# Kernel optimization log

Hardware: AMD Instinct MI355X
Metric: run time of the kernel (lower is better)

The kernel has to match this reference:

```python
import jax, jax.numpy as jnp
import numpy as np

N = 20000
E = 640000
H, C = 4, 64
L = 3
B = 16
EPS = 1e-5


def setup_inputs() -> dict:
    key = jax.random.key(0)
    ks = jax.random.split(key, 12)
    x = jax.random.normal(ks[0], (N, 256), dtype=jnp.float32)
    edge_index = jax.random.randint(ks[1], (2, E), 0, N, dtype=jnp.int64)
    batch = jnp.sort(jax.random.randint(ks[2], (N,), 0, B, dtype=jnp.int64))
    s = 0.05
    return {
        "x": x,
        "edge_index": edge_index,
        "batch": batch,
        "Wl": jax.random.normal(ks[3], (L, 256, H * C), dtype=jnp.float32) * s,
        "bl": jnp.zeros((L, H * C), dtype=jnp.float32),
        "Wr": jax.random.normal(ks[4], (L, 256, H * C), dtype=jnp.float32) * s,
        "br": jnp.zeros((L, H * C), dtype=jnp.float32),
        "att": jax.random.normal(ks[5], (L, H, C), dtype=jnp.float32) * s,
        "conv_bias": jnp.zeros((L, H * C), dtype=jnp.float32),
        "prelu_a": jnp.full((L,), 0.25, dtype=jnp.float32),
        "norm_w": jnp.ones((H * C,), dtype=jnp.float32),
        "norm_b": jnp.zeros((H * C,), dtype=jnp.float32),
        "norm_alpha": jnp.ones((H * C,), dtype=jnp.float32),
        "fc_W": jax.random.normal(ks[6], (H * C, 128), dtype=jnp.float32) * s,
        "fc_b": jnp.zeros((128,), dtype=jnp.float32),
    }


def graph_norm(h, w, b, alpha):
    # GraphNorm with batch=None: all rows form one segment (as in source forward)
    mean = jnp.mean(h, axis=0, keepdims=True)
    shifted = h - alpha * mean
    var = jnp.mean(shifted * shifted, axis=0, keepdims=True)
    return w * shifted / jnp.sqrt(var + EPS) + b


def gatv2_layer(h, src, dst, Wl, bl, Wr, br, att, bias):
    xl = (h @ Wl + bl).reshape(N, H, C)  # source transform
    xr = (h @ Wr + br).reshape(N, H, C)  # target transform
    m = jax.nn.leaky_relu(xl[src] + xr[dst], negative_slope=0.2)  # [Etot,H,C]
    e = jnp.einsum("ehc,hc->eh", m, att)  # [Etot,H]
    emax = jax.ops.segment_max(e, dst, num_segments=N)  # self-loops guarantee coverage
    ex = jnp.exp(e - emax[dst])
    denom = jax.ops.segment_sum(ex, dst, num_segments=N)
    alpha = ex / denom[dst]
    out = jax.ops.segment_sum(alpha[:, :, None] * xl[src], dst, num_segments=N)
    return out.reshape(N, H * C) + bias


def reference(x, edge_index, batch, Wl, bl, Wr, br, att, conv_bias, prelu_a,
              norm_w, norm_b, norm_alpha, fc_W, fc_b):
    loop = jnp.arange(N, dtype=edge_index.dtype)
    src = jnp.concatenate([edge_index[0], loop])  # add self-loops (PyG default)
    dst = jnp.concatenate([edge_index[1], loop])
    h = x
    for l in range(L):
        h = gatv2_layer(h, src, dst, Wl[l], bl[l], Wr[l], br[l], att[l], conv_bias[l])
        h = graph_norm(h, norm_w, norm_b, norm_alpha)
        h = jnp.where(h >= 0, h, prelu_a[l] * h)  # PReLU; dropout is identity in eval
    pooled = jax.ops.segment_sum(h, batch, num_segments=B)  # global_add_pool
    pooled = graph_norm(pooled, norm_w, norm_b, norm_alpha)  # shared norm reused after pool
    return pooled @ fc_W + fc_b
```

## Files before the change

kernel.cpp:

```cpp
#include <hip/hip_runtime.h>
#include <math.h>

#define N_NODES 20000
#define N_EDGES 640000
#define ETOT (N_EDGES + N_NODES)
#define HC 256
#define NLAYER 3
#define NBATCH 16
#define GEPS 1e-5f
#define NSLOT 64
#define L2E 1.44269504f

typedef unsigned short u16;
typedef unsigned int u32;
typedef __attribute__((ext_vector_type(8))) short short8;
typedef __attribute__((ext_vector_type(4))) float floatx4;

__device__ __forceinline__ u16 f2bf(float f) {
    u32 u = __float_as_uint(f);
    u32 r = (u + 0x7FFFu + ((u >> 16) & 1u)) >> 16;
    return (u16)r;
}

__device__ __forceinline__ float4 bf2f4(uint2 u) {
    float4 r;
    r.x = __uint_as_float(u.x << 16);
    r.y = __uint_as_float(u.x & 0xFFFF0000u);
    r.z = __uint_as_float(u.y << 16);
    r.w = __uint_as_float(u.y & 0xFFFF0000u);
    return r;
}

__device__ __forceinline__ float dpp_red16(float x) {
    x += __int_as_float(__builtin_amdgcn_update_dpp(0, __float_as_int(x), 0xB1, 0xF, 0xF, true));
    x += __int_as_float(__builtin_amdgcn_update_dpp(0, __float_as_int(x), 0x4E, 0xF, 0xF, true));
    x += __int_as_float(__builtin_amdgcn_update_dpp(0, __float_as_int(x), 0x141, 0xF, 0xF, true));
    x += __int_as_float(__builtin_amdgcn_update_dpp(0, __float_as_int(x), 0x140, 0xF, 0xF, true));
    return x;
}



__global__ __launch_bounds__(256) void prep(const float* __restrict__ x, u16* __restrict__ xbf,
                                            const float* __restrict__ Wl, const float* __restrict__ Wr,
                                            u16* __restrict__ WT, uint4* __restrict__ zbase, int zq) {
    __shared__ float T[32][33];
    int b = blockIdx.x, tid = threadIdx.x;
    if (b < 1250) {
        int rt = b;
        int wid = tid >> 6, lane = tid & 63;
        int row = rt * 16 + (lane & 15);
        int q8 = (lane >> 4) * 8;
        #pragma unroll
        for (int kk = 0; kk < 2; ++kk) {
            int kt = wid + kk * 4;
            int kcol = kt * 32 + q8;
            const float4* px = (const float4*)(x + (size_t)row * 256 + kcol);
            float4 a = px[0], c = px[1];
            u16 o[8] = {f2bf(a.x), f2bf(a.y), f2bf(a.z), f2bf(a.w),
                        f2bf(c.x), f2bf(c.y), f2bf(c.z), f2bf(c.w)};
            *(uint4*)(xbf + (((size_t)rt * 8 + kt) * 64 + lane) * 8) = *(const uint4*)o;
        }
    } else if (b < 1634) {
        int bi = b - 1250;
        int kb = bi & 7;
        int nb = (bi >> 3) & 15;
        int l = bi >> 7;
        int n0 = nb * 32, k0 = kb * 32;
        const float* W = ((n0 < 256) ? Wl : Wr) + (size_t)l * 65536;
        int nn0 = n0 & 255;
        int tx = tid & 31, ty = tid >> 5;
        #pragma unroll
        for (int i = 0; i < 4; ++i)
            T[ty + i * 8][tx] = W[(size_t)(k0 + ty + i * 8) * 256 + nn0 + tx];
        __syncthreads();
        int lane = tid & 63, jp = (tid >> 6) & 1, cl = tid >> 7;
        int ct = n0 / 16 + cl;
        u16 o4[4];
        #pragma unroll
        for (int jj = 0; jj < 4; ++jj)
            o4[jj] = f2bf(T[(lane >> 4) * 8 + jp * 4 + jj][cl * 16 + (lane & 15)]);
        u16* outw = WT + (size_t)l * 131072;
        *(uint2*)(outw + (((size_t)ct * 8 + kb) * 64 + lane) * 8 + jp * 4) = *(const uint2*)o4;
    } else {
        uint4 z = make_uint4(0, 0, 0, 0);
        for (int i = (b - 1634) * 256 + tid; i < zq; i += 120 * 256) zbase[i] = z;
    }
}


__global__ void count_deg(const int* __restrict__ dst, int* __restrict__ deg) {
    int e = blockIdx.x * 256 + threadIdx.x;
    if (e < N_EDGES) atomicAdd(&deg[dst[e]], 1);
}

__global__ __launch_bounds__(1024) void scan_excl(int* __restrict__ data, int* __restrict__ cursor) {
    __shared__ int wsum[16];
    int t = threadIdx.x, lane = t & 63, wid = t >> 6;
    int i0 = t * 20;
    int d[20];
    int tot = 0;
    #pragma unroll
    for (int j = 0; j < 20; ++j) {
        int i = i0 + j;
        int v = (i < N_NODES) ? (data[i] + 1) : 0;
        d[j] = v;
        tot += v;
    }
    int x = tot;
    #pragma unroll
    for (int off = 1; off < 64; off <<= 1) {
        int tmp = __shfl_up(x, off);
        if (lane >= off) x += tmp;
    }
    if (lane == 63) wsum[wid] = x;
    __syncthreads();
    if (t == 0) {
        int run = 0;
        #pragma unroll
        for (int w = 0; w < 16; ++w) { int tv = wsum[w]; wsum[w] = run; run += tv; }
    }
    __syncthreads();
    int run = wsum[wid] + x - tot;
    #pragma unroll
    for (int j = 0; j < 20; ++j) {
        int i = i0 + j;
        if (i < N_NODES) { data[i] = run; cursor[i] = run; }
        run += d[j];
    }
    if (t == 0) data[N_NODES] = ETOT;
}

__global__ void scatter_edges(const int* __restrict__ src, const int* __restrict__ dst,
                              int* __restrict__ cursor, int* __restrict__ col) {
    int t = blockIdx.x * 256 + threadIdx.x;
    if (t < N_NODES) {
        int p = atomicAdd(&cursor[t], 1);
        col[p] = t;
    } else if (t < N_NODES + N_EDGES) {
        int e = t - N_NODES;
        int p = atomicAdd(&cursor[dst[e]], 1);
        col[p] = src[e];
    }
}


__global__ __launch_bounds__(256, 1) void gemm_mfma(
    const u16* __restrict__ At, const u16* __restrict__ WTt,
    const float* __restrict__ b0, const float* __restrict__ b1,
    u16* __restrict__ xlb, u16* __restrict__ xrb) {
    __shared__ u16 tile[32][520];
    int row0 = blockIdx.x * 64;
    int tid = threadIdx.x;
    int wave = tid >> 6, lane = tid & 63;
    int quad = lane >> 4, l16 = lane & 15;
    int rt0 = row0 >> 4;
    int ct0 = wave * 8;

    floatx4 acc[4][8] = {};
    const u16* pA[4];
    const u16* pB[8];
    #pragma unroll
    for (int mi = 0; mi < 4; ++mi) {
        int rt = min(rt0 + mi, 1249);
        pA[mi] = At + (size_t)rt * 4096 + lane * 8;
    }
    #pragma unroll
    for (int ni = 0; ni < 8; ++ni)
        pB[ni] = WTt + (size_t)(ct0 + ni) * 4096 + lane * 8;

    #pragma unroll
    for (int kt = 0; kt < 8; ++kt) {
        short8 af[4], bf[8];
        #pragma unroll
        for (int mi = 0; mi < 4; ++mi) af[mi] = *(const short8*)(pA[mi] + kt * 512);
        #pragma unroll
        for (int ni = 0; ni < 8; ++ni) bf[ni] = *(const short8*)(pB[ni] + kt * 512);
        #pragma unroll
        for (int mi = 0; mi < 4; ++mi)
            #pragma unroll
            for (int ni = 0; ni < 8; ++ni)
                acc[mi][ni] = __builtin_amdgcn_mfma_f32_16x16x32_bf16(af[mi], bf[ni], acc[mi][ni], 0, 0, 0);
    }

    float bv[8];
    #pragma unroll
    for (int ni = 0; ni < 8; ++ni) {
        int c = wave * 128 + ni * 16 + l16;
        bv[ni] = (c < 256) ? b0[c] : b1[c - 256];
    }

    #pragma unroll
    for (int pass = 0; pass < 2; ++pass) {
        #pragma unroll
        for (int mi = 0; mi < 2; ++mi) {
            int lrow = mi * 16 + quad * 4;
            #pragma unroll
            for (int ni = 0; ni < 8; ++ni) {
                int c = wave * 128 + ni * 16 + l16;
                #pragma unroll
                for (int r = 0; r < 4; ++r)
                    tile[lrow + r][c] = f2bf(acc[pass * 2 + mi][ni][r] + bv[ni]);
            }
        }
        __syncthreads();
        #pragma unroll
        for (int iter = 0; iter < 8; ++iter) {
            int lrow = iter * 4 + wave;
            int gr = row0 + pass * 32 + lrow;
            if (gr < N_NODES) {
                if (lane < 32)
                    *(uint4*)(xlb + (size_t)gr * 256 + lane * 8) = *(const uint4*)&tile[lrow][lane * 8];
                else
                    *(uint4*)(xrb + (size_t)gr * 256 + (lane - 32) * 8) = *(const uint4*)&tile[lrow][256 + (lane - 32) * 8];
            }
        }
        __syncthreads();
    }
}


__global__ __launch_bounds__(256) void gat_agg(
    const u16* __restrict__ xlb, const u16* __restrict__ xrb,
    const int* __restrict__ rowptr, const int* __restrict__ col,
    const float* __restrict__ att_l, const float* __restrict__ bias_l,
    u16* __restrict__ hB, float* __restrict__ slot) {
    __shared__ float sred[4][520];
    int wid = threadIdx.x >> 6, lane = threadIdx.x & 63;
    int node = blockIdx.x * 4 + wid;
    const uint2* xl2 = (const uint2*)xlb;
    float4 attv = ((const float4*)att_l)[lane];
    attv.x *= L2E; attv.y *= L2E; attv.z *= L2E; attv.w *= L2E;
    float4 xrv = bf2f4(((const uint2*)xrb)[(size_t)node * 64 + lane]);
    int beg = rowptr[node], end = rowptr[node + 1];

    float denom = 0.f;
    float4 acc = make_float4(0.f, 0.f, 0.f, 0.f);

    int j = beg;
    for (; j + 8 <= end; j += 8) {
        int s[8];
        uint2 raw[8];
        float4 a[8];
        float p[8];
        #pragma unroll
        for (int u = 0; u < 8; ++u) s[u] = col[j + u];
        #pragma unroll
        for (int u = 0; u < 8; ++u) raw[u] = xl2[(size_t)s[u] * 64 + lane];
        #pragma unroll
        for (int u = 0; u < 8; ++u) {
            a[u] = bf2f4(raw[u]);
            float vx = a[u].x + xrv.x, vy = a[u].y + xrv.y;
            float vz = a[u].z + xrv.z, vw = a[u].w + xrv.w;
            vx = fmaxf(vx, 0.2f * vx);
            vy = fmaxf(vy, 0.2f * vy);
            vz = fmaxf(vz, 0.2f * vz);
            vw = fmaxf(vw, 0.2f * vw);
            p[u] = vx * attv.x + vy * attv.y + vz * attv.z + vw * attv.w;
        }
        #pragma unroll
        for (int u = 0; u < 8; ++u) p[u] = dpp_red16(p[u]);
        #pragma unroll
        for (int u = 0; u < 8; ++u) {
            float w = exp2f(p[u]);
            denom += w;
            acc.x += w * a[u].x; acc.y += w * a[u].y;
            acc.z += w * a[u].z; acc.w += w * a[u].w;
        }
    }
    for (; j < end; ++j) {
        int s = col[j];
        float4 a = bf2f4(xl2[(size_t)s * 64 + lane]);
        float vx = a.x + xrv.x, vy = a.y + xrv.y;
        float vz = a.z + xrv.z, vw = a.w + xrv.w;
        vx = fmaxf(vx, 0.2f * vx);
        vy = fmaxf(vy, 0.2f * vy);
        vz = fmaxf(vz, 0.2f * vz);
        vw = fmaxf(vw, 0.2f * vw);
        float p = vx * attv.x + vy * attv.y + vz * attv.z + vw * attv.w;
        p = dpp_red16(p);
        float w = exp2f(p);
        denom += w;
        acc.x += w * a.x; acc.y += w * a.y; acc.z += w * a.z; acc.w += w * a.w;
    }

    float inv = 1.f / denom;
    float4 b4 = ((const float4*)bias_l)[lane];
    float4 o;
    o.x = acc.x * inv + b4.x; o.y = acc.y * inv + b4.y;
    o.z = acc.z * inv + b4.z; o.w = acc.w * inv + b4.w;
    u16 ob[4] = {f2bf(o.x), f2bf(o.y), f2bf(o.z), f2bf(o.w)};
    ((uint2*)hB)[(size_t)node * 64 + lane] = *(const uint2*)ob;

    int cb2 = lane * 4;
    sred[wid][cb2 + 0] = o.x; sred[wid][cb2 + 1] = o.y;
    sred[wid][cb2 + 2] = o.z; sred[wid][cb2 + 3] = o.w;
    sred[wid][256 + cb2 + 0] = o.x * o.x; sred[wid][256 + cb2 + 1] = o.y * o.y;
    sred[wid][256 + cb2 + 2] = o.z * o.z; sred[wid][256 + cb2 + 3] = o.w * o.w;
    __syncthreads();
    int t = threadIdx.x;
    #pragma unroll
    for (int h = 0; h < 2; ++h) {
        int idx = t + h * 256;
        float s = sred[0][idx] + sred[1][idx] + sred[2][idx] + sred[3][idx];
        atomicAdd(&slot[(blockIdx.x & (NSLOT - 1)) * 512 + idx], s);
    }
}


__global__ __launch_bounds__(256) void fin_stats(const float* __restrict__ slot,
                                                 const float* __restrict__ nw, const float* __restrict__ nb,
                                                 const float* __restrict__ na,
                                                 float* __restrict__ wcbb) {
    int c = threadIdx.x;
    float sum = 0.f, sq = 0.f;
    for (int s = 0; s < NSLOT; ++s) {
        sum += slot[s * 512 + c];
        sq += slot[s * 512 + 256 + c];
    }
    const float invn = 1.f / (float)N_NODES;
    float mean = sum * invn, Eh2 = sq * invn;
    float a = na[c];
    float var = Eh2 - (2.f * a - a * a) * mean * mean;
    float wc = nw[c] * rsqrtf(var + GEPS);
    wcbb[c] = wc;
    wcbb[256 + c] = nb[c] - a * mean * wc;
}


__global__ __launch_bounds__(256) void norm_prelu(const u16* __restrict__ hB, u16* __restrict__ hbfT,
                                                  const float* __restrict__ wcbb,
                                                  const float* __restrict__ pa, int l) {
    int rt = blockIdx.x;
    int wid = threadIdx.x >> 6, lane = threadIdx.x & 63;
    float ap = pa[l];
    int row = rt * 16 + (lane & 15);
    int q8 = (lane >> 4) * 8;
    #pragma unroll
    for (int kk = 0; kk < 2; ++kk) {
        int kt = wid + kk * 4;
        int kcol = kt * 32 + q8;
        uint4 raw = *(const uint4*)(hB + (size_t)row * 256 + kcol);
        float4 a = bf2f4(make_uint2(raw.x, raw.y));
        float4 b = bf2f4(make_uint2(raw.z, raw.w));
        float4 wc0 = *(const float4*)&wcbb[kcol];
        float4 wc1 = *(const float4*)&wcbb[kcol + 4];
        float4 bb0 = *(const float4*)&wcbb[256 + kcol];
        float4 bb1 = *(const float4*)&wcbb[256 + kcol + 4];
        a.x = a.x * wc0.x + bb0.x; a.y = a.y * wc0.y + bb0.y;
        a.z = a.z * wc0.z + bb0.z; a.w = a.w * wc0.w + bb0.w;
        b.x = b.x * wc1.x + bb1.x; b.y = b.y * wc1.y + bb1.y;
        b.z = b.z * wc1.z + bb1.z; b.w = b.w * wc1.w + bb1.w;
        a.x = fmaxf(a.x, ap * a.x); a.y = fmaxf(a.y, ap * a.y);
        a.z = fmaxf(a.z, ap * a.z); a.w = fmaxf(a.w, ap * a.w);
        b.x = fmaxf(b.x, ap * b.x); b.y = fmaxf(b.y, ap * b.y);
        b.z = fmaxf(b.z, ap * b.z); b.w = fmaxf(b.w, ap * b.w);
        u16 o[8] = {f2bf(a.x), f2bf(a.y), f2bf(a.z), f2bf(a.w),
                    f2bf(b.x), f2bf(b.y), f2bf(b.z), f2bf(b.w)};
        *(uint4*)(hbfT + (((size_t)rt * 8 + kt) * 64 + lane) * 8) = *(const uint4*)o;
    }
}


__global__ __launch_bounds__(256) void pool_kernel(const u16* __restrict__ hB,
                                                   const int* __restrict__ batch,
                                                   const float* __restrict__ slots2,
                                                   const float* __restrict__ nw, const float* __restrict__ nb,
                                                   const float* __restrict__ na, const float* __restrict__ pa,
                                                   float* __restrict__ pooled) {
    __shared__ float accs[NBATCH][256];
    int c = threadIdx.x;
    float sum = 0.f, sq = 0.f;
    for (int s = 0; s < NSLOT; ++s) {
        sum += slots2[s * 512 + c];
        sq += slots2[s * 512 + 256 + c];
    }
    const float invn = 1.f / (float)N_NODES;
    float mean = sum * invn, Eh2 = sq * invn;
    float a = na[c];
    float var = Eh2 - (2.f * a - a * a) * mean * mean;
    float wc = nw[c] * rsqrtf(var + GEPS);
    float bb = nb[c] - a * mean * wc;
    float ap = pa[2];

    #pragma unroll
    for (int b = 0; b < NBATCH; ++b) accs[b][c] = 0.f;
    int r0 = blockIdx.x * 100;
    int r1 = min(N_NODES, r0 + 100);
    for (int i = r0; i < r1; ++i) {
        float v = __uint_as_float(((u32)hB[(size_t)i * 256 + c]) << 16);
        v = v * wc + bb;
        v = fmaxf(v, ap * v);
        accs[batch[i]][c] += v;
    }
    int bmin = batch[r0], bmax = batch[r1 - 1];
    for (int b = bmin; b <= bmax; ++b) atomicAdd(&pooled[b * 256 + c], accs[b][c]);
}


__global__ __launch_bounds__(256) void poolnorm_fc(const float* __restrict__ pooled,
                                                   const float* __restrict__ nw, const float* __restrict__ nb,
                                                   const float* __restrict__ na,
                                                   const float* __restrict__ fcW, const float* __restrict__ fcb,
                                                   float* __restrict__ out) {
    __shared__ float pn[256];
    __shared__ float part[128];
    int b = blockIdx.x;
    int c = threadIdx.x;
    float mean = 0.f, sq = 0.f;
    #pragma unroll
    for (int i = 0; i < NBATCH; ++i) {
        float v = pooled[i * 256 + c];
        mean += v; sq += v * v;
    }
    mean *= (1.f / NBATCH); sq *= (1.f / NBATCH);
    float a = na[c];
    float var = sq - (2.f * a - a * a) * mean * mean;
    float wc = nw[c] * rsqrtf(var + GEPS);
    float bb = nb[c] - a * mean * wc;
    pn[c] = pooled[b * 256 + c] * wc + bb;
    __syncthreads();
    int o = c & 127, half = c >> 7;
    float s = 0.f;
    int kbase = half * 128;
    #pragma unroll 8
    for (int k = 0; k < 128; ++k)
        s += pn[kbase + k] * fcW[(kbase + k) * 128 + o];
    if (half == 1) part[o] = s;
    __syncthreads();
    if (half == 0) out[b * 128 + o] = s + part[o] + fcb[o];
}


extern "C" void kernel_launch(void* const* d_in, const int* in_sizes, int n_in,
                              void* d_out, int out_size, void* d_ws, size_t ws_size,
                              hipStream_t stream) {
    const float* x    = (const float*)d_in[0];
    const int*   ei   = (const int*)d_in[1];
    const int*   batch= (const int*)d_in[2];
    const float* Wl   = (const float*)d_in[3];
    const float* bl   = (const float*)d_in[4];
    const float* Wr   = (const float*)d_in[5];
    const float* br   = (const float*)d_in[6];
    const float* att  = (const float*)d_in[7];
    const float* cb   = (const float*)d_in[8];
    const float* pa   = (const float*)d_in[9];
    const float* nw   = (const float*)d_in[10];
    const float* nb   = (const float*)d_in[11];
    const float* na   = (const float*)d_in[12];
    const float* fcW  = (const float*)d_in[13];
    const float* fcb  = (const float*)d_in[14];
    float* out = (float*)d_out;

    char* ws = (char*)d_ws;
    size_t off = 0;
    auto carve = [&](size_t bytes) -> void* {
        void* p = (void*)(ws + off);
        off += (bytes + 255) & ~(size_t)255;
        return p;
    };
    size_t z0 = off;
    int*   rowptr = (int*)carve((N_NODES + 1) * sizeof(int));
    float* slots  = (float*)carve((size_t)NLAYER * NSLOT * 512 * sizeof(float));
    float* pooled = (float*)carve(NBATCH * HC * sizeof(float));
    size_t z1 = off;
    int*   cursor = (int*)carve(N_NODES * sizeof(int));
    int*   colidx = (int*)carve((size_t)ETOT * sizeof(int));
    u16*   xlb    = (u16*)carve((size_t)N_NODES * HC * sizeof(u16));
    u16*   xrb    = (u16*)carve((size_t)N_NODES * HC * sizeof(u16));
    u16*   hB     = (u16*)carve((size_t)N_NODES * HC * sizeof(u16));
    u16*   xbf    = (u16*)carve((size_t)N_NODES * HC * sizeof(u16));
    u16*   hbf    = (u16*)carve((size_t)N_NODES * HC * sizeof(u16));
    u16*   WT     = (u16*)carve((size_t)NLAYER * 512 * 256 * sizeof(u16));
    float* wcbb   = (float*)carve(512 * sizeof(float));

    int zq = (int)((z1 - z0) / 16);
    const int* srcp = ei;
    const int* dstp = ei + N_EDGES;

    prep<<<1754, 256, 0, stream>>>(x, xbf, Wl, Wr, WT, (uint4*)(ws + z0), zq);
    count_deg<<<(N_EDGES + 255) / 256, 256, 0, stream>>>(dstp, rowptr);
    scan_excl<<<1, 1024, 0, stream>>>(rowptr, cursor);
    scatter_edges<<<(ETOT + 255) / 256, 256, 0, stream>>>(srcp, dstp, cursor, colidx);

    for (int l = 0; l < NLAYER; ++l) {
        const u16* Asrc = (l == 0) ? xbf : hbf;
        gemm_mfma<<<313, 256, 0, stream>>>(Asrc, WT + (size_t)l * 131072,
                                           bl + l * 256, br + l * 256, xlb, xrb);
        gat_agg<<<5000, 256, 0, stream>>>(xlb, xrb, rowptr, colidx, att + l * 256, cb + l * 256,
                                          hB, slots + (size_t)l * NSLOT * 512);
        if (l < NLAYER - 1) {
            fin_stats<<<1, 256, 0, stream>>>(slots + (size_t)l * NSLOT * 512, nw, nb, na, wcbb);
            norm_prelu<<<1250, 256, 0, stream>>>(hB, hbf, wcbb, pa, l);
        }
    }
    pool_kernel<<<200, 256, 0, stream>>>(hB, batch, slots + (size_t)2 * NSLOT * 512,
                                         nw, nb, na, pa, pooled);
    poolnorm_fc<<<16, 256, 0, stream>>>(pooled, nw, nb, na, fcW, fcb, out);
}
```

Baseline: 504.1 us.

## Prefetch next edge batch in GAT aggregation, coalesce scan and norm_prelu loads

The gather loop in gat_agg now loads the next 8 neighbor rows while the current 8 are processed, a software double-buffer meant to hide gather latency at the cost of more registers. The single-block scan now walks 1024-element chunks with coalesced accesses and a carried prefix in place of 20 strided elements per thread. norm_prelu stages its 16-row tile in shared memory with coalesced row loads before doing the transposed reads.

```diff
diff --git a/kernel.cpp b/kernel.cpp
--- a/kernel.cpp
+++ b/kernel.cpp
@@ -96,39 +96,35 @@
 
 __global__ __launch_bounds__(1024) void scan_excl(int* __restrict__ data, int* __restrict__ cursor) {
     __shared__ int wsum[16];
-    int t = threadIdx.x, lane = t & 63, wid = t >> 6;
-    int i0 = t * 20;
-    int d[20];
-    int tot = 0;
-    #pragma unroll
-    for (int j = 0; j < 20; ++j) {
-        int i = i0 + j;
+    __shared__ int carry_s;
+    int tid = threadIdx.x, lane = tid & 63, wid = tid >> 6;
+    if (tid == 0) carry_s = 0;
+    __syncthreads();
+    for (int base = 0; base < N_NODES; base += 1024) {
+        int i = base + tid;
         int v = (i < N_NODES) ? (data[i] + 1) : 0;
-        d[j] = v;
-        tot += v;
-    }
-    int x = tot;
-    #pragma unroll
-    for (int off = 1; off < 64; off <<= 1) {
-        int tmp = __shfl_up(x, off);
-        if (lane >= off) x += tmp;
-    }
-    if (lane == 63) wsum[wid] = x;
-    __syncthreads();
-    if (t == 0) {
-        int run = 0;
-        #pragma unroll
-        for (int w = 0; w < 16; ++w) { int tv = wsum[w]; wsum[w] = run; run += tv; }
-    }
-    __syncthreads();
-    int run = wsum[wid] + x - tot;
-    #pragma unroll
-    for (int j = 0; j < 20; ++j) {
-        int i = i0 + j;
-        if (i < N_NODES) { data[i] = run; cursor[i] = run; }
-        run += d[j];
-    }
-    if (t == 0) data[N_NODES] = ETOT;
+        int x = v;
+        #pragma unroll
+        for (int off = 1; off < 64; off <<= 1) {
+            int t = __shfl_up(x, off);
+            if (lane >= off) x += t;
+        }
+        if (lane == 63) wsum[wid] = x;
+        __syncthreads();
+        int carry = carry_s;
+        __syncthreads();
+        if (tid == 0) {
+            int run = 0;
+            #pragma unroll
+            for (int w2 = 0; w2 < 16; ++w2) { int t = wsum[w2]; wsum[w2] = run; run += t; }
+            carry_s = carry + run;
+        }
+        __syncthreads();
+        int excl = carry + wsum[wid] + x - v;
+        if (i < N_NODES) { data[i] = excl; cursor[i] = excl; }
+        __syncthreads();
+    }
+    if (tid == 0) data[N_NODES] = ETOT;
 }
 
 __global__ void scatter_edges(const int* __restrict__ src, const int* __restrict__ dst,
@@ -219,6 +215,32 @@
     }
 }
 
+
+__device__ __forceinline__ void proc8(const uint2* raw, const float4& xrv, const float4& attv,
+                                      float& denom, float4& acc) {
+    float4 a[8];
+    float p[8];
+    #pragma unroll
+    for (int u = 0; u < 8; ++u) {
+        a[u] = bf2f4(raw[u]);
+        float vx = a[u].x + xrv.x, vy = a[u].y + xrv.y;
+        float vz = a[u].z + xrv.z, vw = a[u].w + xrv.w;
+        vx = fmaxf(vx, 0.2f * vx);
+        vy = fmaxf(vy, 0.2f * vy);
+        vz = fmaxf(vz, 0.2f * vz);
+        vw = fmaxf(vw, 0.2f * vw);
+        p[u] = vx * attv.x + vy * attv.y + vz * attv.z + vw * attv.w;
+    }
+    #pragma unroll
+    for (int u = 0; u < 8; ++u) p[u] = dpp_red16(p[u]);
+    #pragma unroll
+    for (int u = 0; u < 8; ++u) {
+        float w = exp2f(p[u]);
+        denom += w;
+        acc.x += w * a[u].x; acc.y += w * a[u].y;
+        acc.z += w * a[u].z; acc.w += w * a[u].w;
+    }
+}
 
 __global__ __launch_bounds__(256) void gat_agg(
     const u16* __restrict__ xlb, const u16* __restrict__ xrb,
@@ -237,36 +259,31 @@
     float denom = 0.f;
     float4 acc = make_float4(0.f, 0.f, 0.f, 0.f);
 
+    int nfull = (end - beg) >> 3;
     int j = beg;
-    for (; j + 8 <= end; j += 8) {
-        int s[8];
+    if (nfull > 0) {
         uint2 raw[8];
-        float4 a[8];
-        float p[8];
-        #pragma unroll
-        for (int u = 0; u < 8; ++u) s[u] = col[j + u];
-        #pragma unroll
-        for (int u = 0; u < 8; ++u) raw[u] = xl2[(size_t)s[u] * 64 + lane];
-        #pragma unroll
-        for (int u = 0; u < 8; ++u) {
-            a[u] = bf2f4(raw[u]);
-            float vx = a[u].x + xrv.x, vy = a[u].y + xrv.y;
-            float vz = a[u].z + xrv.z, vw = a[u].w + xrv.w;
-            vx = fmaxf(vx, 0.2f * vx);
-            vy = fmaxf(vy, 0.2f * vy);
-            vz = fmaxf(vz, 0.2f * vz);
-            vw = fmaxf(vw, 0.2f * vw);
-            p[u] = vx * attv.x + vy * attv.y + vz * attv.z + vw * attv.w;
-        }
-        #pragma unroll
-        for (int u = 0; u < 8; ++u) p[u] = dpp_red16(p[u]);
-        #pragma unroll
-        for (int u = 0; u < 8; ++u) {
-            float w = exp2f(p[u]);
-            denom += w;
-            acc.x += w * a[u].x; acc.y += w * a[u].y;
-            acc.z += w * a[u].z; acc.w += w * a[u].w;
-        }
+        {
+            int sv[8];
+            #pragma unroll
+            for (int u = 0; u < 8; ++u) sv[u] = col[j + u];
+            #pragma unroll
+            for (int u = 0; u < 8; ++u) raw[u] = xl2[(size_t)sv[u] * 64 + lane];
+        }
+        for (int b = 1; b < nfull; ++b) {
+            int s2[8];
+            uint2 raw2[8];
+            #pragma unroll
+            for (int u = 0; u < 8; ++u) s2[u] = col[j + 8 + u];
+            #pragma unroll
+            for (int u = 0; u < 8; ++u) raw2[u] = xl2[(size_t)s2[u] * 64 + lane];
+            proc8(raw, xrv, attv, denom, acc);
+            #pragma unroll
+            for (int u = 0; u < 8; ++u) raw[u] = raw2[u];
+            j += 8;
+        }
+        proc8(raw, xrv, attv, denom, acc);
+        j += 8;
     }
     for (; j < end; ++j) {
         int s = col[j];
@@ -331,16 +348,27 @@
 __global__ __launch_bounds__(256) void norm_prelu(const u16* __restrict__ hB, u16* __restrict__ hbfT,
                                                   const float* __restrict__ wcbb,
                                                   const float* __restrict__ pa, int l) {
+    __shared__ u16 st[16 * 264];
     int rt = blockIdx.x;
-    int wid = threadIdx.x >> 6, lane = threadIdx.x & 63;
+    int t = threadIdx.x;
+    const uint4* srcp = (const uint4*)(hB + (size_t)rt * 4096);
+    #pragma unroll
+    for (int h = 0; h < 2; ++h) {
+        int idx = t + h * 256;
+        uint4 v = srcp[idx];
+        int r = idx >> 5, c = (idx & 31) * 8;
+        *(uint4*)&st[r * 264 + c] = v;
+    }
+    __syncthreads();
+    int wid = t >> 6, lane = t & 63;
     float ap = pa[l];
-    int row = rt * 16 + (lane & 15);
+    int rl = lane & 15;
     int q8 = (lane >> 4) * 8;
     #pragma unroll
     for (int kk = 0; kk < 2; ++kk) {
         int kt = wid + kk * 4;
         int kcol = kt * 32 + q8;
-        uint4 raw = *(const uint4*)(hB + (size_t)row * 256 + kcol);
+        uint4 raw = *(const uint4*)&st[rl * 264 + kcol];
         float4 a = bf2f4(make_uint2(raw.x, raw.y));
         float4 b = bf2f4(make_uint2(raw.z, raw.w));
         float4 wc0 = *(const float4*)&wcbb[kcol];
```

Result: faster. 489.6 us (-2.9%).
